# Kernel optimization log

Hardware: AMD Instinct MI355X
Metric: run time of the kernel (lower is better)

The kernel has to match this reference:

```python
import jax, jax.numpy as jnp
import numpy as np

N = 8192
E = 262144
NEG = 0.2  # leaky_relu negative slope used throughout


def setup_inputs() -> dict:
    key = jax.random.key(0)
    def rn(i, shape, s=0.05):
        return jax.random.normal(jax.random.fold_in(key, i), shape, jnp.float32) * s
    d = {}
    d["x"] = jax.random.normal(jax.random.fold_in(key, 0), (N, 64), jnp.float32)
    d["edge_index"] = jax.random.randint(jax.random.fold_in(key, 1), (2, E), 0, N, dtype=jnp.int32)
    wshapes = {"w0": (64, 256), "as0": (4, 64), "ad0": (4, 64), "r0": (64, 256),
               "w1": (256, 256), "as1": (4, 64), "ad1": (4, 64), "r1": (256, 256),
               "w2": (256, 64), "as2": (1, 64), "ad2": (1, 64), "r2": (256, 64),
               "p0": (256, 64), "p1": (256, 64),
               "qw": (64, 64), "kw": (64, 64), "vw": (64, 64), "ow": (64, 64),
               "m1w": (64, 64), "m2w": (64, 32), "m3w": (32, 10)}
    for i, (nm, sh) in enumerate(wshapes.items()):
        d[nm] = rn(i + 2, sh)
    for nm, dim in [("g0", 256), ("g1", 256), ("g2", 64)]:
        d[nm] = jnp.ones((dim,), jnp.float32)
    for nm, dim in [("be0", 256), ("be1", 256), ("be2", 64), ("b0", 256), ("b1", 256), ("b2", 64),
                    ("qb", 64), ("kb", 64), ("vb", 64), ("ob", 64), ("m1b", 64), ("m2b", 32), ("m3b", 10)]:
        d[nm] = jnp.zeros((dim,), jnp.float32)
    return d


def _forward(edge_index, x, w0, as0, ad0, b0, g0, be0, r0,
             w1, as1, ad1, b1, g1, be1, r1,
             w2, as2, ad2, b2, g2, be2, r2,
             p0, p1, qw, qb, kw, kb, vw, vb, ow, ob,
             m1w, m1b, m2w, m2b, m3w, m3b):
    n = x.shape[0]
    loops = jnp.arange(n, dtype=edge_index.dtype)
    src = jnp.concatenate([edge_index[0], loops])  # add_self_loops=True
    dst = jnp.concatenate([edge_index[1], loops])

    def gat(h, w, a_s, a_d, b, heads):
        hw = (h @ w).reshape(n, heads, 64)  # [N, H, C]
        # PyG GATConv: e_ij = leaky_relu(att_src . h_j + att_dst . h_i), softmax over in-edges of i
        e = jax.nn.leaky_relu(jnp.sum(hw * a_s, -1)[src] + jnp.sum(hw * a_d, -1)[dst], NEG)  # [Etot, H]
        m = jax.ops.segment_max(e, dst, num_segments=n)
        ex = jnp.exp(e - m[dst])
        den = jax.ops.segment_sum(ex, dst, num_segments=n)
        alpha = ex / (den[dst] + 1e-16)
        out = jax.ops.segment_sum(hw[src] * alpha[:, :, None], dst, num_segments=n)
        return out.reshape(n, heads * 64) + b

    def bn(h, g, bta):  # BatchNorm1d, batch statistics (training-mode math)
        mu = jnp.mean(h, 0)
        var = jnp.var(h, 0)
        return (h - mu) * jax.lax.rsqrt(var + 1e-5) * g + bta

    outs = []
    h = x
    for (w, a_s, a_d, b, g, bt, r, heads) in [
            (w0, as0, ad0, b0, g0, be0, r0, 4),
            (w1, as1, ad1, b1, g1, be1, r1, 4),
            (w2, as2, ad2, b2, g2, be2, r2, 1)]:
        res = h @ r
        h = bn(gat(h, w, a_s, a_d, b, heads), g, bt) + res  # shapes always match here
        h = jax.nn.leaky_relu(h, NEG)
        outs.append(h)

    # JumpingKnowledge 'max' after projecting first two layers to hidden dim
    z = jnp.maximum(jnp.maximum(outs[0] @ p0, outs[1] @ p1), outs[2])  # [N, 64]

    # MultiHeadSelfAttention over all nodes (batch=1 implicit), 2 heads, head_dim=32
    q = (z @ qw + qb).reshape(n, 2, 32)
    k = (z @ kw + kb).reshape(n, 2, 32)
    v = (z @ vw + vb).reshape(n, 2, 32)
    attn = jax.nn.softmax(jnp.einsum('nhd,mhd->hnm', q, k) * (32 ** -0.5), axis=-1)
    z = jnp.einsum('hnm,mhd->nhd', attn, v).reshape(n, 64) @ ow + ob

    # MLP head (no data.batch -> GlobalAttention pool skipped)
    z = jax.nn.leaky_relu(z @ m1w + m1b, NEG)
    z = jax.nn.leaky_relu(z @ m2w + m2b, NEG)
    return z @ m3w + m3b


def reference(x, edge_index, w0, as0, ad0, b0, g0, be0, r0,
              w1, as1, ad1, b1, g1, be1, r1,
              w2, as2, ad2, b2, g2, be2, r2,
              p0, p1, qw, qb, kw, kb, vw, vb, ow, ob,
              m1w, m1b, m2w, m2b, m3w, m3b):
    return _forward(edge_index, x, w0, as0, ad0, b0, g0, be0, r0,
                    w1, as1, ad1, b1, g1, be1, r1,
                    w2, as2, ad2, b2, g2, be2, r2,
                    p0, p1, qw, qb, kw, kb, vw, vb, ow, ob,
                    m1w, m1b, m2w, m2b, m3w, m3b)
```

## Files before the change

kernel.cpp:

```cpp
#include <hip/hip_runtime.h>
#include <hip/hip_bf16.h>


#define NEG 0.2f
#define LOG2E 1.4426950408889634f

__device__ __forceinline__ float leaky(float v) { return v > 0.f ? v : NEG * v; }

__device__ __forceinline__ unsigned bf16u(float x) {
    unsigned u = __float_as_uint(x);
    u += 0x7FFFu + ((u >> 16) & 1u);
    return u >> 16;
}
__device__ __forceinline__ unsigned fmap(float f) {
    unsigned u = __float_as_uint(f);
    return (u & 0x80000000u) ? ~u : (u | 0x80000000u);
}
__device__ __forceinline__ float funmap(unsigned u) {
    unsigned b = (u & 0x80000000u) ? (u & 0x7FFFFFFFu) : ~u;
    return __uint_as_float(b);
}
__device__ __forceinline__ float fexp2(float x) {
#if __has_builtin(__builtin_amdgcn_exp2f)
    return __builtin_amdgcn_exp2f(x);
#else
    return exp2f(x);
#endif
}
__device__ __forceinline__ unsigned cvtpk(float lo, float hi) {
    unsigned r;
    asm("v_cvt_pk_bf16_f32 %0, %1, %2" : "=v"(r) : "v"(lo), "v"(hi));
    return r;
}

typedef __attribute__((ext_vector_type(8))) short bf16x8;
typedef __attribute__((ext_vector_type(16))) float f32x16;
typedef __attribute__((ext_vector_type(4))) unsigned uint4v;

__device__ __forceinline__ void split1(float v, unsigned& hb, unsigned& lb) {
    hb = bf16u(v);
    float hf = __uint_as_float(hb << 16);
    lb = bf16u(v - hf);
}

__global__ void split_rows(const float* __restrict__ in,
                           unsigned short* __restrict__ hi,
                           unsigned short* __restrict__ lo, int total4)
{
    int i = blockIdx.x * 256 + threadIdx.x;
    if (i >= total4) return;
    float4 v = ((const float4*)in)[i];
    float vv[4] = {v.x, v.y, v.z, v.w};
    ushort4 h, l;
#pragma unroll
    for (int j = 0; j < 4; ++j) {
        unsigned hb, lb;
        split1(vv[j], hb, lb);
        (&h.x)[j] = (unsigned short)hb;
        (&l.x)[j] = (unsigned short)lb;
    }
    ((ushort4*)hi)[i] = h;
    ((ushort4*)lo)[i] = l;
}

struct WEnt { const float* src; unsigned short* hi; unsigned short* lo; int K; int N; };
struct WArr { WEnt e[15]; };

__global__ void split_weights(WArr a)
{
    WEnt w = a.e[blockIdx.y];
    int id = blockIdx.x * 256 + threadIdx.x;
    if (id >= w.K * w.N) return;
    int k = id / w.N, n = id - k * w.N;
    unsigned hb, lb;
    split1(w.src[id], hb, lb);
    w.hi[(size_t)n * w.K + k] = (unsigned short)hb;
    w.lo[(size_t)n * w.K + k] = (unsigned short)lb;
}

__global__ __launch_bounds__(256) void gemm_mfma(
    const unsigned short* __restrict__ Ahi, const unsigned short* __restrict__ Alo,
    const unsigned short* __restrict__ Bhi, const unsigned short* __restrict__ Blo,
    const float* __restrict__ bias, float* __restrict__ C,
    unsigned short* __restrict__ Chi, unsigned short* __restrict__ Clo,
    int M, int N, int K, int act)
{
    const int lane = threadIdx.x & 63, wid = threadIdx.x >> 6;
    const int hb4 = lane >> 5, lq = lane & 31;
    const int row0 = blockIdx.y * 64 + (wid >> 1) * 32;
    const int col0 = blockIdx.x * 64 + (wid & 1) * 32;
    const size_t abase = (size_t)(row0 + lq) * K + hb4 * 8;
    const size_t bbase = (size_t)(col0 + lq) * K + hb4 * 8;
    f32x16 acc0, acc1;
#pragma unroll
    for (int r = 0; r < 16; ++r) { acc0[r] = 0.f; acc1[r] = 0.f; }
    for (int k0 = 0; k0 < K; k0 += 16) {
        bf16x8 a_h = *(const bf16x8*)(Ahi + abase + k0);
        bf16x8 a_l = *(const bf16x8*)(Alo + abase + k0);
        bf16x8 b_h = *(const bf16x8*)(Bhi + bbase + k0);
        bf16x8 b_l = *(const bf16x8*)(Blo + bbase + k0);
        acc0 = __builtin_amdgcn_mfma_f32_32x32x16_bf16(a_h, b_h, acc0, 0, 0, 0);
        acc1 = __builtin_amdgcn_mfma_f32_32x32x16_bf16(a_l, b_h, acc1, 0, 0, 0);
        acc1 = __builtin_amdgcn_mfma_f32_32x32x16_bf16(a_h, b_l, acc1, 0, 0, 0);
    }
    int col = col0 + lq;
    if (col >= N) return;
    float bs = bias ? bias[col] : 0.f;
#pragma unroll
    for (int r = 0; r < 16; ++r) {
        int row = row0 + (r & 3) + 8 * (r >> 2) + 4 * hb4;
        float v = acc0[r] + acc1[r] + bs;
        if (act) v = leaky(v);
        C[(size_t)row * N + col] = v;
        if (Chi) {
            unsigned hh, ll;
            split1(v, hh, ll);
            Chi[(size_t)row * N + col] = (unsigned short)hh;
            Clo[(size_t)row * N + col] = (unsigned short)ll;
        }
    }
}

template <int H>
__global__ __launch_bounds__(256) void sd_kernel(
    const float* __restrict__ hwres, int S,
    const float* __restrict__ a_s, const float* __restrict__ a_d,
    float* __restrict__ sval, float* __restrict__ dval,
    unsigned* __restrict__ svmax, int Nn)
{
    int i = blockIdx.x * 256 + threadIdx.x;
    int n = i / H, h = i & (H - 1);
    const float4* row = (const float4*)(hwres + (size_t)n * S + h * 64);
    const float4* as4 = (const float4*)(a_s + h * 64);
    const float4* ad4 = (const float4*)(a_d + h * 64);
    float s = 0.f, d = 0.f;
#pragma unroll
    for (int c = 0; c < 16; ++c) {
        float4 x = row[c], a = as4[c], b = ad4[c];
        s += x.x * a.x + x.y * a.y + x.z * a.z + x.w * a.w;
        d += x.x * b.x + x.y * b.y + x.z * b.z + x.w * b.w;
    }
    s *= LOG2E;
    d *= LOG2E;
    sval[i] = s;
    dval[i] = d;
    float m = s;
#pragma unroll
    for (int off = H; off < 64; off <<= 1) m = fmaxf(m, __shfl_xor(m, off));
    if ((threadIdx.x & 63) < H) atomicMax(&svmax[h], fmap(m));
}

__global__ void csr_count(const int* __restrict__ ei, int* __restrict__ cnt, int E) {
    int i = blockIdx.x * 256 + threadIdx.x;
    if (i < E) atomicAdd(&cnt[ei[E + i]], 1);
}

__global__ __launch_bounds__(256) void csr_scan(const int* __restrict__ cnt,
                                                int* __restrict__ rowptr,
                                                int* __restrict__ fill, int Nn)
{
    __shared__ int part[256];
    int t = threadIdx.x;
    int loc[32];
    int s = 0;
#pragma unroll
    for (int j = 0; j < 32; ++j) { loc[j] = s; s += cnt[t * 32 + j]; }
    part[t] = s;
    __syncthreads();
    for (int d = 1; d < 256; d <<= 1) {
        int v = (t >= d) ? part[t - d] : 0;
        __syncthreads();
        part[t] += v;
        __syncthreads();
    }
    int off = (t > 0) ? part[t - 1] : 0;
#pragma unroll
    for (int j = 0; j < 32; ++j) {
        int v = off + loc[j];
        rowptr[t * 32 + j] = v;
        fill[t * 32 + j] = v;
    }
    if (t == 255) rowptr[Nn] = part[255];
}

__global__ void csr_scatter(const int* __restrict__ ei, int* __restrict__ fill,
                            int* __restrict__ srcidx, int E) {
    int i = blockIdx.x * 256 + threadIdx.x;
    if (i < E) {
        int d = ei[E + i];
        int p = atomicAdd(&fill[d], 1);
        srcidx[p] = ei[i];
    }
}

__global__ __launch_bounds__(256) void gat_gather4(
    const int* __restrict__ rowptr, const int* __restrict__ srcidx,
    const float* __restrict__ hwres, int S,
    const float* __restrict__ sval, const float* __restrict__ dval,
    const unsigned* __restrict__ svmax, float* __restrict__ gout, int Nn)
{
    const int node = blockIdx.x * 4 + (threadIdx.x >> 6);
    const int lane = threadIdx.x & 63;
    const int hd = lane >> 4;
    const int cb = lane * 4;
    const int beg = rowptr[node], end = rowptr[node + 1];
    const float dv = dval[node * 4 + hd];
    const float B = leaky(funmap(svmax[hd]) + dv);
    float p = fexp2(leaky(sval[node * 4 + hd] + dv) - B);
    float l = p;
    float4 hv = *(const float4*)(hwres + (size_t)node * S + cb);
    float a0 = p * hv.x, a1 = p * hv.y, a2 = p * hv.z, a3 = p * hv.w;
    int i = beg;
    for (; i + 2 <= end; i += 2) {
        int s0 = srcidx[i], s1 = srcidx[i + 1];
        float p0 = fexp2(leaky(sval[s0 * 4 + hd] + dv) - B);
        float p1 = fexp2(leaky(sval[s1 * 4 + hd] + dv) - B);
        float4 r0 = *(const float4*)(hwres + (size_t)s0 * S + cb);
        float4 r1 = *(const float4*)(hwres + (size_t)s1 * S + cb);
        l += p0 + p1;
        a0 += p0 * r0.x + p1 * r1.x;
        a1 += p0 * r0.y + p1 * r1.y;
        a2 += p0 * r0.z + p1 * r1.z;
        a3 += p0 * r0.w + p1 * r1.w;
    }
    if (i < end) {
        int s0 = srcidx[i];
        float p0 = fexp2(leaky(sval[s0 * 4 + hd] + dv) - B);
        float4 r0 = *(const float4*)(hwres + (size_t)s0 * S + cb);
        l += p0;
        a0 += p0 * r0.x; a1 += p0 * r0.y; a2 += p0 * r0.z; a3 += p0 * r0.w;
    }
    float inv = 1.f / l;
    *(float4*)(gout + (size_t)node * 256 + cb) =
        make_float4(a0 * inv, a1 * inv, a2 * inv, a3 * inv);
}

__global__ __launch_bounds__(256) void gat_gather1(
    const int* __restrict__ rowptr, const int* __restrict__ srcidx,
    const float* __restrict__ hwres, int S,
    const float* __restrict__ sval, const float* __restrict__ dval,
    const unsigned* __restrict__ svmax, float* __restrict__ gout, int Nn)
{
    const int node = blockIdx.x * 4 + (threadIdx.x >> 6);
    const int lane = threadIdx.x & 63;
    const int beg = rowptr[node], end = rowptr[node + 1];
    const float dv = dval[node];
    const float B = leaky(funmap(svmax[0]) + dv);
    float p = fexp2(leaky(sval[node] + dv) - B);
    float l = p;
    float acc = p * hwres[(size_t)node * S + lane];
    int i = beg;
    for (; i + 2 <= end; i += 2) {
        int s0 = srcidx[i], s1 = srcidx[i + 1];
        float p0 = fexp2(leaky(sval[s0] + dv) - B);
        float p1 = fexp2(leaky(sval[s1] + dv) - B);
        l += p0 + p1;
        acc += p0 * hwres[(size_t)s0 * S + lane] + p1 * hwres[(size_t)s1 * S + lane];
    }
    if (i < end) {
        int s0 = srcidx[i];
        float p0 = fexp2(leaky(sval[s0] + dv) - B);
        l += p0;
        acc += p0 * hwres[(size_t)s0 * S + lane];
    }
    gout[(size_t)node * 64 + lane] = acc / l;
}

__global__ void bn_partial(const float* __restrict__ gout, double* __restrict__ sums,
                           int Nn, int C)
{
    int t = threadIdx.x;
    int c = t % C, sub = t / C, nsub = blockDim.x / C;
    int rbase = blockIdx.x * 32;
    double s = 0.0, sq = 0.0;
    for (int r = rbase + sub; r < rbase + 32; r += nsub) {
        float x = gout[(size_t)r * C + c];
        s += x;
        sq += (double)x * x;
    }
    atomicAdd(&sums[c], s);
    atomicAdd(&sums[C + c], sq);
}

__global__ void bn_finalize(const double* __restrict__ sums, float* __restrict__ mu,
                            float* __restrict__ rstd, int Nn, int C)
{
    int c = threadIdx.x;
    if (c >= C) return;
    double m = sums[c] / Nn;
    double v = sums[C + c] / Nn - m * m;
    mu[c] = (float)m;
    rstd[c] = (float)(1.0 / sqrt(v + 1e-5));
}

__global__ void bn_res_act(const float* __restrict__ gout,
                           const float* __restrict__ hwres, int S, int logC,
                           const float* __restrict__ mu, const float* __restrict__ rstd,
                           const float* __restrict__ g, const float* __restrict__ be,
                           float* __restrict__ outp,
                           unsigned short* __restrict__ shi,
                           unsigned short* __restrict__ slo, int total)
{
    int i = blockIdx.x * blockDim.x + threadIdx.x;
    if (i >= total) return;
    int C = 1 << logC;
    int c = i & (C - 1), row = i >> logC;
    float v = (gout[i] - mu[c]) * rstd[c] * g[c] + be[c]
              + hwres[(size_t)row * S + C + c];
    v = leaky(v);
    if (outp) outp[i] = v;
    if (shi) {
        unsigned hb, lb;
        split1(v, hb, lb);
        shi[i] = (unsigned short)hb;
        slo[i] = (unsigned short)lb;
    }
}

__global__ void jk_max(const float* __restrict__ a, const float* __restrict__ b,
                       const float* __restrict__ c,
                       unsigned short* __restrict__ shi,
                       unsigned short* __restrict__ slo, int total)
{
    int i = blockIdx.x * blockDim.x + threadIdx.x;
    if (i >= total) return;
    float v = fmaxf(fmaxf(a[i], b[i]), c[i]);
    unsigned hb, lb;
    split1(v, hb, lb);
    shi[i] = (unsigned short)hb;
    slo[i] = (unsigned short)lb;
}

__global__ void kmax_kernel(const float* __restrict__ zqkv,
                            const float* __restrict__ kb,
                            unsigned* __restrict__ kmax, int N)
{
    const int c = threadIdx.x & 63, g = threadIdx.x >> 6;
    const int rows = N / (gridDim.x * 4);
    const int r0 = (blockIdx.x * 4 + g) * rows;
    float bc = kb[c];
    float m = 0.f;
    for (int r = r0; r < r0 + rows; ++r)
        m = fmaxf(m, fabsf(zqkv[(size_t)r * 192 + 64 + c] + bc));
    atomicMax(&kmax[c], __float_as_uint(m));
}

__global__ void qk_prep(const float* __restrict__ zqkv,
                        const float* __restrict__ qb, const float* __restrict__ kb,
                        const unsigned* __restrict__ kmaxu,
                        __hip_bfloat16* __restrict__ Qb, __hip_bfloat16* __restrict__ Kb,
                        float* __restrict__ bound, int N)
{
    int idx = blockIdx.x * 256 + threadIdx.x;
    if (idx >= 2 * N) return;
    int h = idx / N, row = idx - h * N;
    const float scale = 0.17677669529663687f * LOG2E;
    const float* qp = zqkv + (size_t)row * 192 + h * 32;
    const float* kp = zqkv + (size_t)row * 192 + 64 + h * 32;
    float b = 0.f;
    unsigned qo[16], ko[16];
#pragma unroll
    for (int i = 0; i < 16; ++i) {
        float q0 = (qp[2 * i] + qb[h * 32 + 2 * i]) * scale;
        float q1 = (qp[2 * i + 1] + qb[h * 32 + 2 * i + 1]) * scale;
        float k0 = kp[2 * i] + kb[h * 32 + 2 * i];
        float k1 = kp[2 * i + 1] + kb[h * 32 + 2 * i + 1];
        b += fabsf(q0) * __uint_as_float(kmaxu[h * 32 + 2 * i]);
        b += fabsf(q1) * __uint_as_float(kmaxu[h * 32 + 2 * i + 1]);
        qo[i] = bf16u(q0) | (bf16u(q1) << 16);
        ko[i] = bf16u(k0) | (bf16u(k1) << 16);
    }
    uint4* qd = (uint4*)(Qb + (size_t)idx * 32);
    uint4* kd = (uint4*)(Kb + (size_t)idx * 32);
#pragma unroll
    for (int i = 0; i < 4; ++i) {
        qd[i] = make_uint4(qo[4 * i], qo[4 * i + 1], qo[4 * i + 2], qo[4 * i + 3]);
        kd[i] = make_uint4(ko[4 * i], ko[4 * i + 1], ko[4 * i + 2], ko[4 * i + 3]);
    }
    bound[idx] = b;
}

__global__ void v_prep(const float* __restrict__ zqkv, const float* __restrict__ vb,
                       __hip_bfloat16* __restrict__ Vf, int N)
{
    int idx = blockIdx.x * 256 + threadIdx.x;
    int total = 2 * (N >> 4) * 64;
    if (idx >= total) return;
    int lane = idx & 63;
    int g = (idx >> 6) % (N >> 4);
    int h = (idx >> 6) / (N >> 4);
    int kb_ = g * 16 + (lane >> 5) * 8;
    int d = (lane & 31) + h * 32;
    float bd = vb[d];
    unsigned o[4];
#pragma unroll
    for (int i = 0; i < 4; ++i) {
        unsigned u0 = bf16u(zqkv[(size_t)(kb_ + 2 * i) * 192 + 128 + d] + bd);
        unsigned u1 = bf16u(zqkv[(size_t)(kb_ + 2 * i + 1) * 192 + 128 + d] + bd);
        o[i] = u0 | (u1 << 16);
    }
    *(uint4*)(Vf + (size_t)idx * 8) = make_uint4(o[0], o[1], o[2], o[3]);
}

__global__ __launch_bounds__(256) void attn_mfma(
    const __hip_bfloat16* __restrict__ Qb, const __hip_bfloat16* __restrict__ Kb,
    const __hip_bfloat16* __restrict__ Vf, const float* __restrict__ bound,
    float* __restrict__ pl, __hip_bfloat16* __restrict__ pacc,
    int N, int nchunk, int chunksz)
{
    const int lane = threadIdx.x & 63;
    const int wid = threadIdx.x >> 6;
    const int hi = lane >> 5, lq = lane & 31;
    const int chunk = blockIdx.x;
    const int qtile = blockIdx.y * 4 + wid;
    const int head = qtile / (N >> 5);
    const int q0 = (qtile % (N >> 5)) * 32;
    const int kbase = chunk * chunksz;

    const size_t qrow = (size_t)head * N + q0 + lq;
    const bf16x8 qf0 = *(const bf16x8*)(Qb + qrow * 32 + hi * 8);
    const bf16x8 qf1 = *(const bf16x8*)(Qb + qrow * 32 + hi * 8 + 16);
    const float bnd = bound[qrow];

    f32x16 oacc;
#pragma unroll
    for (int r = 0; r < 16; ++r) oacc[r] = 0.f;
    float lsum = 0.f;

    for (int kt = kbase; kt < kbase + chunksz; kt += 32) {
        const size_t krow = (size_t)head * N + kt + lq;
        const bf16x8 kf0 = *(const bf16x8*)(Kb + krow * 32 + hi * 8);
        const bf16x8 kf1 = *(const bf16x8*)(Kb + krow * 32 + hi * 8 + 16);
        f32x16 s;
#pragma unroll
        for (int r = 0; r < 16; ++r) s[r] = 0.f;
        s = __builtin_amdgcn_mfma_f32_32x32x16_bf16(kf0, qf0, s, 0, 0, 0);
        s = __builtin_amdgcn_mfma_f32_32x32x16_bf16(kf1, qf1, s, 0, 0, 0);
        const __hip_bfloat16* vfb =
            Vf + (((size_t)head * (N >> 4) + (kt >> 4)) * 64 + lane) * 8;
        const bf16x8 vf0 = *(const bf16x8*)vfb;
        const bf16x8 vf1 = *(const bf16x8*)(vfb + 64 * 8);

        float p[16];
#pragma unroll
        for (int r = 0; r < 16; ++r) p[r] = fexp2(s[r] - bnd);
        float ls = 0.f;
#pragma unroll
        for (int r = 0; r < 16; ++r) ls += p[r];
        lsum += ls;

        unsigned wpk[8];
#pragma unroll
        for (int i = 0; i < 8; ++i) wpk[i] = cvtpk(p[2 * i], p[2 * i + 1]);
        unsigned wsx[8];
#pragma unroll
        for (int i = 0; i < 8; ++i) wsx[i] = (unsigned)__shfl_xor((int)wpk[i], 32);
        uint4v b1, b2;
        b1[0] = hi ? wsx[2] : wpk[0];
        b1[1] = hi ? wsx[3] : wpk[1];
        b1[2] = hi ? wpk[2] : wsx[0];
        b1[3] = hi ? wpk[3] : wsx[1];
        b2[0] = hi ? wsx[6] : wpk[4];
        b2[1] = hi ? wsx[7] : wpk[5];
        b2[2] = hi ? wpk[6] : wsx[4];
        b2[3] = hi ? wpk[7] : wsx[5];
        oacc = __builtin_amdgcn_mfma_f32_32x32x16_bf16(
            vf0, __builtin_bit_cast(bf16x8, b1), oacc, 0, 0, 0);
        oacc = __builtin_amdgcn_mfma_f32_32x32x16_bf16(
            vf1, __builtin_bit_cast(bf16x8, b2), oacc, 0, 0, 0);
    }
    lsum += __shfl_xor(lsum, 32);
    const size_t hr = (size_t)head * N + q0 + lq;
    if (hi == 0) pl[hr * nchunk + chunk] = lsum;
    __hip_bfloat16* pb = pacc + (hr * nchunk + chunk) * 32;
#pragma unroll
    for (int rg = 0; rg < 4; ++rg) {
        unsigned lo = cvtpk(oacc[rg * 4 + 0], oacc[rg * 4 + 1]);
        unsigned hw2 = cvtpk(oacc[rg * 4 + 2], oacc[rg * 4 + 3]);
        *(uint2*)(pb + rg * 8 + hi * 4) = make_uint2(lo, hw2);
    }
}

__global__ void attn_combine(const float* __restrict__ pl,
                             const __hip_bfloat16* __restrict__ pacc,
                             unsigned short* __restrict__ shi,
                             unsigned short* __restrict__ slo, int N, int nchunk)
{
    int i = blockIdx.x * blockDim.x + threadIdx.x;
    if (i >= 2 * N * 32) return;
    int hr = i >> 5, cc = i & 31;
    float l = 0.f, a = 0.f;
    for (int c = 0; c < nchunk; ++c) {
        l += pl[(size_t)hr * nchunk + c];
        a += __bfloat162float(pacc[((size_t)hr * nchunk + c) * 32 + cc]);
    }
    int head = hr / N, row = hr - head * N;
    float v = a / l;
    size_t oi = (size_t)row * 64 + head * 32 + cc;
    unsigned hb, lb;
    split1(v, hb, lb);
    shi[oi] = (unsigned short)hb;
    slo[oi] = (unsigned short)lb;
}

extern "C" void kernel_launch(void* const* d_in, const int* in_sizes, int n_in,
                              void* d_out, int out_size, void* d_ws, size_t ws_size,
                              hipStream_t stream)
{
    const float* x = (const float*)d_in[0];
    const int* ei = (const int*)d_in[1];
    const float* w[3]   = {(const float*)d_in[2], (const float*)d_in[6],  (const float*)d_in[10]};
    const float* as_[3] = {(const float*)d_in[3], (const float*)d_in[7],  (const float*)d_in[11]};
    const float* ad_[3] = {(const float*)d_in[4], (const float*)d_in[8],  (const float*)d_in[12]};
    const float* rw[3]  = {(const float*)d_in[5], (const float*)d_in[9],  (const float*)d_in[13]};
    const float* p0 = (const float*)d_in[14];
    const float* p1 = (const float*)d_in[15];
    const float* qw = (const float*)d_in[16];
    const float* kw = (const float*)d_in[17];
    const float* vw = (const float*)d_in[18];
    const float* ow = (const float*)d_in[19];
    const float* m1w = (const float*)d_in[20];
    const float* m2w = (const float*)d_in[21];
    const float* m3w = (const float*)d_in[22];
    const float* g_[3]  = {(const float*)d_in[23], (const float*)d_in[24], (const float*)d_in[25]};
    const float* be_[3] = {(const float*)d_in[26], (const float*)d_in[27], (const float*)d_in[28]};
    const float* qb  = (const float*)d_in[32];
    const float* kb  = (const float*)d_in[33];
    const float* vb  = (const float*)d_in[34];
    const float* ob  = (const float*)d_in[35];
    const float* m1b = (const float*)d_in[36];
    const float* m2b = (const float*)d_in[37];
    const float* m3b = (const float*)d_in[38];

    const int N = in_sizes[0] / 64;
    const int E = in_sizes[1] / 2;

    float* ws = (float*)d_ws;
    size_t off = 0;
    auto alloc = [&](size_t n) {
        float* p = ws + off;
        off += (n + 255) & ~(size_t)255;
        return p;
    };
    float* hwres = alloc((size_t)N * 512);
    float* gout  = alloc((size_t)N * 256);
    unsigned short* sChi = (unsigned short*)alloc((size_t)N * 128);
    unsigned short* sClo = (unsigned short*)alloc((size_t)N * 128);
    float* h2   = alloc((size_t)N * 64);
    float* sval = alloc((size_t)N * 4);
    float* dval = alloc((size_t)N * 4);
    float* mu   = alloc(256);
    float* rstd = alloc(256);
    size_t ms_begin = off;
    int* cnt = (int*)alloc(N);
    double* bnsum = (double*)alloc(3 * 1024);
    unsigned* kmaxu = (unsigned*)alloc(64);
    unsigned* svmax = (unsigned*)alloc(16);
    size_t ms_end = off;
    int* rowptr = (int*)alloc(N + 256);
    int* fill   = (int*)alloc(N);
    int* srcidx = (int*)alloc(E);
    unsigned short* sAhi = (unsigned short*)alloc((size_t)N * 128);
    unsigned short* sAlo = (unsigned short*)alloc((size_t)N * 128);
    unsigned short* sBhi = (unsigned short*)alloc((size_t)N * 32);
    unsigned short* sBlo = (unsigned short*)alloc((size_t)N * 32);
    unsigned short* G0h = (unsigned short*)alloc(512 * 64 / 2);
    unsigned short* G0l = (unsigned short*)alloc(512 * 64 / 2);
    unsigned short* G1h = (unsigned short*)alloc(512 * 256 / 2);
    unsigned short* G1l = (unsigned short*)alloc(512 * 256 / 2);
    unsigned short* G2h = (unsigned short*)alloc(128 * 256 / 2);
    unsigned short* G2l = (unsigned short*)alloc(128 * 256 / 2);
    unsigned short* P0h = (unsigned short*)alloc(64 * 256 / 2);
    unsigned short* P0l = (unsigned short*)alloc(64 * 256 / 2);
    unsigned short* P1h = (unsigned short*)alloc(64 * 256 / 2);
    unsigned short* P1l = (unsigned short*)alloc(64 * 256 / 2);
    unsigned short* Gqh = (unsigned short*)alloc(192 * 64 / 2);
    unsigned short* Gql = (unsigned short*)alloc(192 * 64 / 2);
    unsigned short* Owh = (unsigned short*)alloc(64 * 64 / 2);
    unsigned short* Owl = (unsigned short*)alloc(64 * 64 / 2);
    unsigned short* M1h = (unsigned short*)alloc(64 * 64 / 2);
    unsigned short* M1l = (unsigned short*)alloc(64 * 64 / 2);
    unsigned short* M2h = (unsigned short*)alloc(64 * 64 / 2);
    unsigned short* M2l = (unsigned short*)alloc(64 * 64 / 2);
    unsigned short* M3h = (unsigned short*)alloc(64 * 32 / 2);
    unsigned short* M3l = (unsigned short*)alloc(64 * 32 / 2);
    float* zqkv = hwres;
    __hip_bfloat16* pacc = (__hip_bfloat16*)(hwres + (size_t)N * 192);
    float* tA = gout;
    float* tB = gout + (size_t)N * 64;
    float* tC = gout + 2 * (size_t)N * 64;
    const int NCHUNK = 8;
    __hip_bfloat16* Qb = (__hip_bfloat16*)sChi;
    __hip_bfloat16* Kb = Qb + (size_t)2 * N * 32;
    __hip_bfloat16* Vf = Kb + (size_t)2 * N * 32;
    float* boundArr = (float*)(Vf + (size_t)2 * N * 32);
    float* pl = h2;

    {
        WArr wa;
        wa.e[0]  = WEnt{w[0],  G0h,              G0l,              64, 256};
        wa.e[1]  = WEnt{rw[0], G0h + 256 * 64,   G0l + 256 * 64,   64, 256};
        wa.e[2]  = WEnt{w[1],  G1h,              G1l,              256, 256};
        wa.e[3]  = WEnt{rw[1], G1h + 256 * 256,  G1l + 256 * 256,  256, 256};
        wa.e[4]  = WEnt{w[2],  G2h,              G2l,              256, 64};
        wa.e[5]  = WEnt{rw[2], G2h + 64 * 256,   G2l + 64 * 256,   256, 64};
        wa.e[6]  = WEnt{p0,    P0h,              P0l,              256, 64};
        wa.e[7]  = WEnt{p1,    P1h,              P1l,              256, 64};
        wa.e[8]  = WEnt{qw,    Gqh,              Gql,              64, 64};
        wa.e[9]  = WEnt{kw,    Gqh + 64 * 64,    Gql + 64 * 64,    64, 64};
        wa.e[10] = WEnt{vw,    Gqh + 128 * 64,   Gql + 128 * 64,   64, 64};
        wa.e[11] = WEnt{ow,    Owh,              Owl,              64, 64};
        wa.e[12] = WEnt{m1w,   M1h,              M1l,              64, 64};
        wa.e[13] = WEnt{m2w,   M2h,              M2l,              64, 32};
        wa.e[14] = WEnt{m3w,   M3h,              M3l,              32, 10};
        split_weights<<<dim3(256, 15), 256, 0, stream>>>(wa);
    }
    hipMemsetAsync(ws + ms_begin, 0, (ms_end - ms_begin) * 4, stream);
    csr_count<<<(E + 255) / 256, 256, 0, stream>>>(ei, cnt, E);
    csr_scan<<<1, 256, 0, stream>>>(cnt, rowptr, fill, N);
    csr_scatter<<<(E + 255) / 256, 256, 0, stream>>>(ei, fill, srcidx, E);
    split_rows<<<(N * 64 / 4 + 255) / 256, 256, 0, stream>>>(x, sAhi, sAlo, N * 64 / 4);

    auto gemmM = [&](const unsigned short* Ah, const unsigned short* Al,
                     const unsigned short* Bh, const unsigned short* Bl,
                     const float* bias, float* C, unsigned short* Chi,
                     unsigned short* Clo, int M, int Nc, int K, int act) {
        dim3 grid((Nc + 63) / 64, M / 64);
        gemm_mfma<<<grid, 256, 0, stream>>>(Ah, Al, Bh, Bl, bias, C, Chi, Clo,
                                            M, Nc, K, act);
    };

    const unsigned short* inh[3] = {sAhi, sChi, sAhi};
    const unsigned short* inl[3] = {sAlo, sClo, sAlo};
    unsigned short* outh[3] = {sChi, sAhi, nullptr};
    unsigned short* outl[3] = {sClo, sAlo, nullptr};
    const unsigned short* Gh[3] = {G0h, G1h, G2h};
    const unsigned short* Gl[3] = {G0l, G1l, G2l};
    int Ksz[3] = {64, 256, 256}, Csz[3] = {256, 256, 64}, logC[3] = {8, 8, 6};
    int Hh[3] = {4, 4, 1};

    for (int l = 0; l < 3; ++l) {
        int C = Csz[l], S = 2 * C;
        gemmM(inh[l], inl[l], Gh[l], Gl[l], nullptr, hwres, nullptr, nullptr,
              N, S, Ksz[l], 0);
        if (Hh[l] == 4) {
            sd_kernel<4><<<N * 4 / 256, 256, 0, stream>>>(
                hwres, S, as_[l], ad_[l], sval, dval, svmax + l * 4, N);
            gat_gather4<<<N / 4, 256, 0, stream>>>(
                rowptr, srcidx, hwres, S, sval, dval, svmax + l * 4, gout, N);
        } else {
            sd_kernel<1><<<N / 256, 256, 0, stream>>>(
                hwres, S, as_[l], ad_[l], sval, dval, svmax + l * 4, N);
            gat_gather1<<<N / 4, 256, 0, stream>>>(
                rowptr, srcidx, hwres, S, sval, dval, svmax + l * 4, gout, N);
        }
        double* bns = bnsum + l * 512;
        bn_partial<<<N / 32, 256, 0, stream>>>(gout, bns, N, C);
        bn_finalize<<<1, 256, 0, stream>>>(bns, mu, rstd, N, C);
        bn_res_act<<<((size_t)N * C) / 256, 256, 0, stream>>>(
            gout, hwres, S, logC[l], mu, rstd, g_[l], be_[l],
            l == 2 ? h2 : nullptr, outh[l], outl[l], N * C);
    }

    gemmM(sChi, sClo, P0h, P0l, nullptr, tA, nullptr, nullptr, N, 64, 256, 0);
    gemmM(sAhi, sAlo, P1h, P1l, nullptr, tB, nullptr, nullptr, N, 64, 256, 0);
    jk_max<<<((size_t)N * 64) / 256, 256, 0, stream>>>(tA, tB, h2, sBhi, sBlo, N * 64);

    gemmM(sBhi, sBlo, Gqh, Gql, nullptr, zqkv, nullptr, nullptr, N, 192, 64, 0);

    kmax_kernel<<<32, 256, 0, stream>>>(zqkv, kb, kmaxu, N);
    qk_prep<<<(2 * N + 255) / 256, 256, 0, stream>>>(zqkv, qb, kb, kmaxu, Qb, Kb, boundArr, N);
    v_prep<<<(2 * (N >> 4) * 64 + 255) / 256, 256, 0, stream>>>(zqkv, vb, Vf, N);
    attn_mfma<<<dim3(NCHUNK, (2 * N / 32) / 4), 256, 0, stream>>>(
        Qb, Kb, Vf, boundArr, pl, pacc, N, NCHUNK, N / NCHUNK);
    attn_combine<<<(2 * N * 32 + 255) / 256, 256, 0, stream>>>(
        pl, pacc, sAhi, sAlo, N, NCHUNK);

    gemmM(sAhi, sAlo, Owh, Owl, ob, tA, sBhi, sBlo, N, 64, 64, 0);
    gemmM(sBhi, sBlo, M1h, M1l, m1b, tB, sAhi, sAlo, N, 64, 64, 1);
    gemmM(sAhi, sAlo, M2h, M2l, m2b, tC, sBhi, sBlo, N, 32, 64, 1);
    gemmM(sBhi, sBlo, M3h, M3l, m3b, (float*)d_out, nullptr, nullptr, N, 10, 32, 0);
}
```

Baseline: 391.7 us.

## Fuse JK max, kmax, BN finalize, QKV prep and MLP head into fewer kernels

Measured after the change: 403.1 us. 1.03x slower.

```diff
diff --git a/kernel.cpp b/kernel.cpp
--- a/kernel.cpp
+++ b/kernel.cpp
@@ -83,6 +83,8 @@
     const unsigned short* __restrict__ Bhi, const unsigned short* __restrict__ Blo,
     const float* __restrict__ bias, float* __restrict__ C,
     unsigned short* __restrict__ Chi, unsigned short* __restrict__ Clo,
+    const float* __restrict__ jkB, const float* __restrict__ jkC,
+    unsigned* __restrict__ kmaxDst, const float* __restrict__ kbias,
     int M, int N, int K, int act)
 {
     const int lane = threadIdx.x & 63, wid = threadIdx.x >> 6;
@@ -106,12 +108,16 @@
     int col = col0 + lq;
     if (col >= N) return;
     float bs = bias ? bias[col] : 0.f;
+    float kmx = 0.f;
 #pragma unroll
     for (int r = 0; r < 16; ++r) {
         int row = row0 + (r & 3) + 8 * (r >> 2) + 4 * hb4;
         float v = acc0[r] + acc1[r] + bs;
         if (act) v = leaky(v);
-        C[(size_t)row * N + col] = v;
+        if (jkB) v = fmaxf(fmaxf(v, jkB[(size_t)row * N + col]),
+                           jkC[(size_t)row * N + col]);
+        if (kmaxDst) kmx = fmaxf(kmx, fabsf(v + kbias[col & 63]));
+        if (C) C[(size_t)row * N + col] = v;
         if (Chi) {
             unsigned hh, ll;
             split1(v, hh, ll);
@@ -119,6 +125,8 @@
             Clo[(size_t)row * N + col] = (unsigned short)ll;
         }
     }
+    if (kmaxDst && col >= 64 && col < 128)
+        atomicMax(&kmaxDst[col - 64], __float_as_uint(kmx));
 }
 
 template <int H>
@@ -282,20 +290,9 @@
     atomicAdd(&sums[C + c], sq);
 }
 
-__global__ void bn_finalize(const double* __restrict__ sums, float* __restrict__ mu,
-                            float* __restrict__ rstd, int Nn, int C)
-{
-    int c = threadIdx.x;
-    if (c >= C) return;
-    double m = sums[c] / Nn;
-    double v = sums[C + c] / Nn - m * m;
-    mu[c] = (float)m;
-    rstd[c] = (float)(1.0 / sqrt(v + 1e-5));
-}
-
 __global__ void bn_res_act(const float* __restrict__ gout,
                            const float* __restrict__ hwres, int S, int logC,
-                           const float* __restrict__ mu, const float* __restrict__ rstd,
+                           const double* __restrict__ bnsum, double invN,
                            const float* __restrict__ g, const float* __restrict__ be,
                            float* __restrict__ outp,
                            unsigned short* __restrict__ shi,
@@ -305,7 +302,11 @@
     if (i >= total) return;
     int C = 1 << logC;
     int c = i & (C - 1), row = i >> logC;
-    float v = (gout[i] - mu[c]) * rstd[c] * g[c] + be[c]
+    double m = bnsum[c] * invN;
+    double var = bnsum[C + c] * invN - m * m;
+    float mu = (float)m;
+    float rstd = (float)(1.0 / sqrt(var + 1e-5));
+    float v = (gout[i] - mu) * rstd * g[c] + be[c]
               + hwres[(size_t)row * S + C + c];
     v = leaky(v);
     if (outp) outp[i] = v;
@@ -317,89 +318,61 @@
     }
 }
 
-__global__ void jk_max(const float* __restrict__ a, const float* __restrict__ b,
-                       const float* __restrict__ c,
-                       unsigned short* __restrict__ shi,
-                       unsigned short* __restrict__ slo, int total)
-{
-    int i = blockIdx.x * blockDim.x + threadIdx.x;
-    if (i >= total) return;
-    float v = fmaxf(fmaxf(a[i], b[i]), c[i]);
-    unsigned hb, lb;
-    split1(v, hb, lb);
-    shi[i] = (unsigned short)hb;
-    slo[i] = (unsigned short)lb;
-}
-
-__global__ void kmax_kernel(const float* __restrict__ zqkv,
-                            const float* __restrict__ kb,
-                            unsigned* __restrict__ kmax, int N)
-{
-    const int c = threadIdx.x & 63, g = threadIdx.x >> 6;
-    const int rows = N / (gridDim.x * 4);
-    const int r0 = (blockIdx.x * 4 + g) * rows;
-    float bc = kb[c];
-    float m = 0.f;
-    for (int r = r0; r < r0 + rows; ++r)
-        m = fmaxf(m, fabsf(zqkv[(size_t)r * 192 + 64 + c] + bc));
-    atomicMax(&kmax[c], __float_as_uint(m));
-}
-
-__global__ void qk_prep(const float* __restrict__ zqkv,
-                        const float* __restrict__ qb, const float* __restrict__ kb,
-                        const unsigned* __restrict__ kmaxu,
-                        __hip_bfloat16* __restrict__ Qb, __hip_bfloat16* __restrict__ Kb,
-                        float* __restrict__ bound, int N)
+__global__ void qkv_prep(const float* __restrict__ zqkv,
+                         const float* __restrict__ qb, const float* __restrict__ kb,
+                         const float* __restrict__ vb,
+                         const unsigned* __restrict__ kmaxu,
+                         __hip_bfloat16* __restrict__ Qb, __hip_bfloat16* __restrict__ Kb,
+                         __hip_bfloat16* __restrict__ Vf, float* __restrict__ bound,
+                         int N)
 {
     int idx = blockIdx.x * 256 + threadIdx.x;
-    if (idx >= 2 * N) return;
-    int h = idx / N, row = idx - h * N;
-    const float scale = 0.17677669529663687f * LOG2E;
-    const float* qp = zqkv + (size_t)row * 192 + h * 32;
-    const float* kp = zqkv + (size_t)row * 192 + 64 + h * 32;
-    float b = 0.f;
-    unsigned qo[16], ko[16];
-#pragma unroll
-    for (int i = 0; i < 16; ++i) {
-        float q0 = (qp[2 * i] + qb[h * 32 + 2 * i]) * scale;
-        float q1 = (qp[2 * i + 1] + qb[h * 32 + 2 * i + 1]) * scale;
-        float k0 = kp[2 * i] + kb[h * 32 + 2 * i];
-        float k1 = kp[2 * i + 1] + kb[h * 32 + 2 * i + 1];
-        b += fabsf(q0) * __uint_as_float(kmaxu[h * 32 + 2 * i]);
-        b += fabsf(q1) * __uint_as_float(kmaxu[h * 32 + 2 * i + 1]);
-        qo[i] = bf16u(q0) | (bf16u(q1) << 16);
-        ko[i] = bf16u(k0) | (bf16u(k1) << 16);
-    }
-    uint4* qd = (uint4*)(Qb + (size_t)idx * 32);
-    uint4* kd = (uint4*)(Kb + (size_t)idx * 32);
-#pragma unroll
-    for (int i = 0; i < 4; ++i) {
-        qd[i] = make_uint4(qo[4 * i], qo[4 * i + 1], qo[4 * i + 2], qo[4 * i + 3]);
-        kd[i] = make_uint4(ko[4 * i], ko[4 * i + 1], ko[4 * i + 2], ko[4 * i + 3]);
-    }
-    bound[idx] = b;
-}
-
-__global__ void v_prep(const float* __restrict__ zqkv, const float* __restrict__ vb,
-                       __hip_bfloat16* __restrict__ Vf, int N)
-{
-    int idx = blockIdx.x * 256 + threadIdx.x;
-    int total = 2 * (N >> 4) * 64;
-    if (idx >= total) return;
-    int lane = idx & 63;
-    int g = (idx >> 6) % (N >> 4);
-    int h = (idx >> 6) / (N >> 4);
-    int kb_ = g * 16 + (lane >> 5) * 8;
-    int d = (lane & 31) + h * 32;
-    float bd = vb[d];
-    unsigned o[4];
-#pragma unroll
-    for (int i = 0; i < 4; ++i) {
-        unsigned u0 = bf16u(zqkv[(size_t)(kb_ + 2 * i) * 192 + 128 + d] + bd);
-        unsigned u1 = bf16u(zqkv[(size_t)(kb_ + 2 * i + 1) * 192 + 128 + d] + bd);
-        o[i] = u0 | (u1 << 16);
-    }
-    *(uint4*)(Vf + (size_t)idx * 8) = make_uint4(o[0], o[1], o[2], o[3]);
+    if (idx < 2 * N) {
+        int h = idx / N, row = idx - h * N;
+        const float scale = 0.17677669529663687f * LOG2E;
+        const float* qp = zqkv + (size_t)row * 192 + h * 32;
+        const float* kp = zqkv + (size_t)row * 192 + 64 + h * 32;
+        float b = 0.f;
+        unsigned qo[16], ko[16];
+#pragma unroll
+        for (int i = 0; i < 16; ++i) {
+            float q0 = (qp[2 * i] + qb[h * 32 + 2 * i]) * scale;
+            float q1 = (qp[2 * i + 1] + qb[h * 32 + 2 * i + 1]) * scale;
+            float k0 = kp[2 * i] + kb[h * 32 + 2 * i];
+            float k1 = kp[2 * i + 1] + kb[h * 32 + 2 * i + 1];
+            b += fabsf(q0) * __uint_as_float(kmaxu[h * 32 + 2 * i]);
+            b += fabsf(q1) * __uint_as_float(kmaxu[h * 32 + 2 * i + 1]);
+            qo[i] = bf16u(q0) | (bf16u(q1) << 16);
+            ko[i] = bf16u(k0) | (bf16u(k1) << 16);
+        }
+        uint4* qd = (uint4*)(Qb + (size_t)idx * 32);
+        uint4* kd = (uint4*)(Kb + (size_t)idx * 32);
+#pragma unroll
+        for (int i = 0; i < 4; ++i) {
+            qd[i] = make_uint4(qo[4 * i], qo[4 * i + 1], qo[4 * i + 2], qo[4 * i + 3]);
+            kd[i] = make_uint4(ko[4 * i], ko[4 * i + 1], ko[4 * i + 2], ko[4 * i + 3]);
+        }
+        bound[idx] = b;
+    } else {
+        int j = idx - 2 * N;
+        if (j >= 2 * (N >> 4) * 64) return;
+        int lane = j & 63;
+        int g = (j >> 6) % (N >> 4);
+        int h = (j >> 6) / (N >> 4);
+        int hi = lane >> 5;
+        int kbase = g * 16 + 4 * hi;
+        int d = (lane & 31) + h * 32;
+        float bd = vb[d];
+        unsigned o[4];
+#pragma unroll
+        for (int i = 0; i < 4; ++i) {
+            int r0 = kbase + ((2 * i) & 3) + 8 * (i >> 1);
+            unsigned u0 = bf16u(zqkv[(size_t)r0 * 192 + 128 + d] + bd);
+            unsigned u1 = bf16u(zqkv[(size_t)(r0 + 1) * 192 + 128 + d] + bd);
+            o[i] = u0 | (u1 << 16);
+        }
+        *(uint4*)(Vf + (size_t)j * 8) = make_uint4(o[0], o[1], o[2], o[3]);
+    }
 }
 
 __global__ __launch_bounds__(256) void attn_mfma(
@@ -449,21 +422,15 @@
         for (int r = 0; r < 16; ++r) ls += p[r];
         lsum += ls;
 
-        unsigned wpk[8];
-#pragma unroll
-        for (int i = 0; i < 8; ++i) wpk[i] = cvtpk(p[2 * i], p[2 * i + 1]);
-        unsigned wsx[8];
-#pragma unroll
-        for (int i = 0; i < 8; ++i) wsx[i] = (unsigned)__shfl_xor((int)wpk[i], 32);
         uint4v b1, b2;
-        b1[0] = hi ? wsx[2] : wpk[0];
-        b1[1] = hi ? wsx[3] : wpk[1];
-        b1[2] = hi ? wpk[2] : wsx[0];
-        b1[3] = hi ? wpk[3] : wsx[1];
-        b2[0] = hi ? wsx[6] : wpk[4];
-        b2[1] = hi ? wsx[7] : wpk[5];
-        b2[2] = hi ? wpk[6] : wsx[4];
-        b2[3] = hi ? wpk[7] : wsx[5];
+        b1[0] = cvtpk(p[0], p[1]);
+        b1[1] = cvtpk(p[2], p[3]);
+        b1[2] = cvtpk(p[4], p[5]);
+        b1[3] = cvtpk(p[6], p[7]);
+        b2[0] = cvtpk(p[8], p[9]);
+        b2[1] = cvtpk(p[10], p[11]);
+        b2[2] = cvtpk(p[12], p[13]);
+        b2[3] = cvtpk(p[14], p[15]);
         oacc = __builtin_amdgcn_mfma_f32_32x32x16_bf16(
             vf0, __builtin_bit_cast(bf16x8, b1), oacc, 0, 0, 0);
         oacc = __builtin_amdgcn_mfma_f32_32x32x16_bf16(
@@ -481,26 +448,97 @@
     }
 }
 
-__global__ void attn_combine(const float* __restrict__ pl,
-                             const __hip_bfloat16* __restrict__ pacc,
-                             unsigned short* __restrict__ shi,
-                             unsigned short* __restrict__ slo, int N, int nchunk)
-{
-    int i = blockIdx.x * blockDim.x + threadIdx.x;
-    if (i >= 2 * N * 32) return;
-    int hr = i >> 5, cc = i & 31;
-    float l = 0.f, a = 0.f;
-    for (int c = 0; c < nchunk; ++c) {
-        l += pl[(size_t)hr * nchunk + c];
-        a += __bfloat162float(pacc[((size_t)hr * nchunk + c) * 32 + cc]);
-    }
-    int head = hr / N, row = hr - head * N;
-    float v = a / l;
-    size_t oi = (size_t)row * 64 + head * 32 + cc;
-    unsigned hb, lb;
-    split1(v, hb, lb);
-    shi[oi] = (unsigned short)hb;
-    slo[oi] = (unsigned short)lb;
+__global__ __launch_bounds__(256) void mlp_fused(
+    const float* __restrict__ pl, const __hip_bfloat16* __restrict__ pacc,
+    const unsigned short* __restrict__ Owh, const unsigned short* __restrict__ Owl,
+    const float* __restrict__ ob,
+    const unsigned short* __restrict__ M1h, const unsigned short* __restrict__ M1l,
+    const float* __restrict__ m1b,
+    const unsigned short* __restrict__ M2h, const unsigned short* __restrict__ M2l,
+    const float* __restrict__ m2b,
+    const unsigned short* __restrict__ M3h, const unsigned short* __restrict__ M3l,
+    const float* __restrict__ m3b,
+    float* __restrict__ out, int N, int nchunk)
+{
+    __shared__ __align__(16) unsigned short Shi[64][72];
+    __shared__ __align__(16) unsigned short Slo[64][72];
+    const int t = threadIdx.x;
+    const int row0 = blockIdx.x * 64;
+#pragma unroll
+    for (int i = 0; i < 16; ++i) {
+        int idx = i * 256 + t;
+        int row = idx >> 6, ch = idx & 63;
+        int head = ch >> 5, cc = ch & 31;
+        size_t hr = (size_t)head * N + row0 + row;
+        float l = 0.f, a = 0.f;
+        for (int c = 0; c < nchunk; ++c) {
+            l += pl[hr * nchunk + c];
+            a += __bfloat162float(pacc[(hr * nchunk + c) * 32 + cc]);
+        }
+        float v = a / l;
+        unsigned hb, lb;
+        split1(v, hb, lb);
+        Shi[row][ch] = (unsigned short)hb;
+        Slo[row][ch] = (unsigned short)lb;
+    }
+    __syncthreads();
+
+    const int lane = t & 63, wid = t >> 6;
+    const int hb4 = lane >> 5, lq = lane & 31;
+    const int rowb = (wid >> 1) * 32, colb = (wid & 1) * 32;
+    const unsigned short* Wh[4] = {Owh, M1h, M2h, M3h};
+    const unsigned short* Wl[4] = {Owl, M1l, M2l, M3l};
+    const float* Wb[4] = {ob, m1b, m2b, m3b};
+    const int Ncs[4] = {64, 64, 32, 10};
+    const int Kcs[4] = {64, 64, 64, 32};
+    const int actf[4] = {0, 1, 1, 0};
+
+#pragma unroll
+    for (int s = 0; s < 4; ++s) {
+        const int Nc = Ncs[s], K = Kcs[s];
+        const int col = colb + lq;
+        const bool active = colb < Nc;
+        f32x16 acc0, acc1;
+#pragma unroll
+        for (int r = 0; r < 16; ++r) { acc0[r] = 0.f; acc1[r] = 0.f; }
+        if (active) {
+            for (int k0 = 0; k0 < K; k0 += 16) {
+                bf16x8 a_h = *(const bf16x8*)&Shi[rowb + lq][k0 + hb4 * 8];
+                bf16x8 a_l = *(const bf16x8*)&Slo[rowb + lq][k0 + hb4 * 8];
+                bf16x8 b_h = *(const bf16x8*)&Wh[s][(size_t)col * K + k0 + hb4 * 8];
+                bf16x8 b_l = *(const bf16x8*)&Wl[s][(size_t)col * K + k0 + hb4 * 8];
+                acc0 = __builtin_amdgcn_mfma_f32_32x32x16_bf16(a_h, b_h, acc0, 0, 0, 0);
+                acc1 = __builtin_amdgcn_mfma_f32_32x32x16_bf16(a_l, b_h, acc1, 0, 0, 0);
+                acc1 = __builtin_amdgcn_mfma_f32_32x32x16_bf16(a_h, b_l, acc1, 0, 0, 0);
+            }
+        }
+        __syncthreads();
+        if (s == 3) {
+            if (active && col < 10) {
+#pragma unroll
+                for (int r = 0; r < 16; ++r) {
+                    int row = rowb + (r & 3) + 8 * (r >> 2) + 4 * hb4;
+                    out[(size_t)(row0 + row) * 10 + col] =
+                        acc0[r] + acc1[r] + m3b[col];
+                }
+            }
+        } else {
+            if (active) {
+                float bs = Wb[s][col];
+#pragma unroll
+                for (int r = 0; r < 16; ++r) {
+                    int row = rowb + (r & 3) + 8 * (r >> 2) + 4 * hb4;
+                    float v = acc0[r] + acc1[r] + bs;
+                    if (actf[s]) v = leaky(v);
+                    unsigned hb, lb;
+                    split1(v, hb, lb);
+                    Shi[row][col] = (unsigned short)hb;
+                    Slo[row][col] = (unsigned short)lb;
+                }
+            }
+            __syncthreads();
+        }
+    }
 }
 
 extern "C" void kernel_launch(void* const* d_in, const int* in_sizes, int n_in,
@@ -549,8 +587,6 @@
     float* h2   = alloc((size_t)N * 64);
     float* sval = alloc((size_t)N * 4);
     float* dval = alloc((size_t)N * 4);
-    float* mu   = alloc(256);
-    float* rstd = alloc(256);
     size_t ms_begin = off;
     int* cnt = (int*)alloc(N);
     double* bnsum = (double*)alloc(3 * 1024);
@@ -586,9 +622,7 @@
     unsigned short* M3l = (unsigned short*)alloc(64 * 32 / 2);
     float* zqkv = hwres;
     __hip_bfloat16* pacc = (__hip_bfloat16*)(hwres + (size_t)N * 192);
-    float* tA = gout;
-    float* tB = gout + (size_t)N * 64;
-    float* tC = gout + 2 * (size_t)N * 64;
+    float* tB = gout;
     const int NCHUNK = 8;
     __hip_bfloat16* Qb = (__hip_bfloat16*)sChi;
     __hip_bfloat16* Kb = Qb + (size_t)2 * N * 32;
@@ -624,10 +658,12 @@
     auto gemmM = [&](const unsigned short* Ah, const unsigned short* Al,
                      const unsigned short* Bh, const unsigned short* Bl,
                      const float* bias, float* C, unsigned short* Chi,
-                     unsigned short* Clo, int M, int Nc, int K, int act) {
+                     unsigned short* Clo, const float* jkB, const float* jkC,
+                     unsigned* kmx, const float* kbias,
+                     int M, int Nc, int K, int act) {
         dim3 grid((Nc + 63) / 64, M / 64);
         gemm_mfma<<<grid, 256, 0, stream>>>(Ah, Al, Bh, Bl, bias, C, Chi, Clo,
-                                            M, Nc, K, act);
+                                            jkB, jkC, kmx, kbias, M, Nc, K, act);
     };
 
     const unsigned short* inh[3] = {sAhi, sChi, sAhi};
@@ -642,7 +678,7 @@
     for (int l = 0; l < 3; ++l) {
         int C = Csz[l], S = 2 * C;
         gemmM(inh[l], inl[l], Gh[l], Gl[l], nullptr, hwres, nullptr, nullptr,
-              N, S, Ksz[l], 0);
+              nullptr, nullptr, nullptr, nullptr, N, S, Ksz[l], 0);
         if (Hh[l] == 4) {
             sd_kernel<4><<<N * 4 / 256, 256, 0, stream>>>(
                 hwres, S, as_[l], ad_[l], sval, dval, svmax + l * 4, N);
@@ -656,28 +692,26 @@
         }
         double* bns = bnsum + l * 512;
         bn_partial<<<N / 32, 256, 0, stream>>>(gout, bns, N, C);
-        bn_finalize<<<1, 256, 0, stream>>>(bns, mu, rstd, N, C);
         bn_res_act<<<((size_t)N * C) / 256, 256, 0, stream>>>(
-            gout, hwres, S, logC[l], mu, rstd, g_[l], be_[l],
+            gout, hwres, S, logC[l], bns, 1.0 / (double)N, g_[l], be_[l],
             l == 2 ? h2 : nullptr, outh[l], outl[l], N * C);
     }
 
-    gemmM(sChi, sClo, P0h, P0l, nullptr, tA, nullptr, nullptr, N, 64, 256, 0);
-    gemmM(sAhi, sAlo, P1h, P1l, nullptr, tB, nullptr, nullptr, N, 64, 256, 0);
-    jk_max<<<((size_t)N * 64) / 256, 256, 0, stream>>>(tA, tB, h2, sBhi, sBlo, N * 64);
-
-    gemmM(sBhi, sBlo, Gqh, Gql, nullptr, zqkv, nullptr, nullptr, N, 192, 64, 0);
-
-    kmax_kernel<<<32, 256, 0, stream>>>(zqkv, kb, kmaxu, N);
-    qk_prep<<<(2 * N + 255) / 256, 256, 0, stream>>>(zqkv, qb, kb, kmaxu, Qb, Kb, boundArr, N);
-    v_prep<<<(2 * (N >> 4) * 64 + 255) / 256, 256, 0, stream>>>(zqkv, vb, Vf, N);
+    gemmM(sAhi, sAlo, P1h, P1l, nullptr, tB, nullptr, nullptr,
+          nullptr, nullptr, nullptr, nullptr, N, 64, 256, 0);
+    gemmM(sChi, sClo, P0h, P0l, nullptr, nullptr, sBhi, sBlo,
+          tB, h2, nullptr, nullptr, N, 64, 256, 0);
+
+    gemmM(sBhi, sBlo, Gqh, Gql, nullptr, zqkv, nullptr, nullptr,
+          nullptr, nullptr, kmaxu, kb, N, 192, 64, 0);
+
+    int ptot = 2 * N + 2 * (N >> 4) * 64;
+    qkv_prep<<<(ptot + 255) / 256, 256, 0, stream>>>(
+        zqkv, qb, kb, vb, kmaxu, Qb, Kb, Vf, boundArr, N);
     attn_mfma<<<dim3(NCHUNK, (2 * N / 32) / 4), 256, 0, stream>>>(
         Qb, Kb, Vf, boundArr, pl, pacc, N, NCHUNK, N / NCHUNK);
-    attn_combine<<<(2 * N * 32 + 255) / 256, 256, 0, stream>>>(
-        pl, pacc, sAhi, sAlo, N, NCHUNK);
-
-    gemmM(sAhi, sAlo, Owh, Owl, ob, tA, sBhi, sBlo, N, 64, 64, 0);
-    gemmM(sBhi, sBlo, M1h, M1l, m1b, tB, sAhi, sAlo, N, 64, 64, 1);
-    gemmM(sAhi, sAlo, M2h, M2l, m2b, tC, sBhi, sBlo, N, 32, 64, 1);
-    gemmM(sBhi, sBlo, M3h, M3l, m3b, (float*)d_out, nullptr, nullptr, N, 10, 32, 0);
-}
+
+    mlp_fused<<<N / 64, 256, 0, stream>>>(
+        pl, pacc, Owh, Owl, ob, M1h, M1l, m1b, M2h, M2l, m2b,
+        M3h, M3l, m3b, (float*)d_out, N, NCHUNK);
+}
```
